# Kernel optimization log

Hardware: AMD Instinct MI355X
Metric: run time of the kernel (lower is better)

The kernel has to match this reference:

```python
import jax, jax.numpy as jnp
import numpy as np

N_NODES = 100000
N_EDGES = 640000
NIN = 128
NOUT = 128


def setup_inputs() -> dict:
    key = jax.random.key(0)
    ks = jax.random.split(key, 10)
    scale = 1.0 / np.sqrt(NIN)
    x = jax.random.normal(ks[0], (N_NODES, NIN), dtype=jnp.float32)
    edge_index = jax.random.randint(ks[1], (2, N_EDGES), 0, N_NODES, dtype=jnp.int64)
    edge_attr = jnp.zeros((N_EDGES, 1), dtype=jnp.float32)
    Wk = jax.random.uniform(ks[2], (NIN, NOUT), jnp.float32, -scale, scale)
    bk = jax.random.uniform(ks[3], (NOUT,), jnp.float32, -scale, scale)
    Wq = jax.random.uniform(ks[4], (NIN, NOUT), jnp.float32, -scale, scale)
    bq = jax.random.uniform(ks[5], (NOUT,), jnp.float32, -scale, scale)
    Wv = jax.random.uniform(ks[6], (NIN, NOUT), jnp.float32, -scale, scale)
    bv = jax.random.uniform(ks[7], (NOUT,), jnp.float32, -scale, scale)
    Wskip = jax.random.uniform(ks[8], (NIN, NOUT), jnp.float32, -scale, scale)
    bias = jax.random.uniform(ks[9], (NOUT,), jnp.float32, -scale, scale)
    return {
        "x": x, "edge_index": edge_index, "edge_attr": edge_attr,
        "Wk": Wk, "bk": bk, "Wq": Wq, "bq": bq,
        "Wv": Wv, "bv": bv, "Wskip": Wskip, "bias": bias,
    }


def reference(x, edge_index, edge_attr, Wk, bk, Wq, bq, Wv, bv, Wskip, bias):
    # PyG ResGatedGraphConv: out_i = W_skip x_i + b + sum_{j->i} sigmoid(k_i + q_j) * v_j
    # k = lin_key(x) (applied to dst), q = lin_query(x) (src), v = lin_value(x) (src)
    src, dst = edge_index[0], edge_index[1]
    k = x @ Wk + bk            # [N, NOUT]
    q = x @ Wq + bq            # [N, NOUT]
    v = x @ Wv + bv            # [N, NOUT]
    eta = jax.nn.sigmoid(k[dst] + q[src])   # [E, NOUT] per-edge gate
    msg = eta * v[src]                       # [E, NOUT]
    agg = jax.ops.segment_sum(msg, dst, num_segments=x.shape[0])  # [N, NOUT]
    return agg + x @ Wskip + bias
```

## Files before the change

### kernel.cpp

```cpp
#include <hip/hip_runtime.h>
#include <hip/hip_bf16.h>

typedef __bf16 v4bf __attribute__((ext_vector_type(4)));
typedef __bf16 v8bf __attribute__((ext_vector_type(8)));
typedef float  v16f __attribute__((ext_vector_type(16)));

__device__ __forceinline__ unsigned short f2bf(float f) {
    union { float f; unsigned int u; } a; a.f = f;
    unsigned int r = a.u + 0x7FFFu + ((a.u >> 16) & 1u);
    return (unsigned short)(r >> 16);
}

__device__ __forceinline__ void unpack8(uint4 rawv, float* f) {
    unsigned int w[4] = { rawv.x, rawv.y, rawv.z, rawv.w };
    #pragma unroll
    for (int i = 0; i < 4; ++i) {
        f[2 * i]     = __uint_as_float(w[i] << 16);
        f[2 * i + 1] = __uint_as_float(w[i] & 0xFFFF0000u);
    }
}

__global__ __launch_bounds__(256) void prep_w(
    const float* __restrict__ Wk, const float* __restrict__ Wq,
    const float* __restrict__ Wv, const float* __restrict__ Ws,
    unsigned short* __restrict__ Wt)
{
    int i = blockIdx.x * 256 + threadIdx.x;
    int m = i >> 14;
    int r = i & 16383;
    int n = r >> 7, k = r & 127;
    const float* W = (m == 0) ? Wk : (m == 1) ? Wq : (m == 2) ? Wv : Ws;
    Wt[i] = f2bf(W[k * 128 + n]);
}

__global__ __launch_bounds__(256) void gemm_one(
    const float* __restrict__ x, int N,
    const unsigned short* __restrict__ Wt,
    const float* __restrict__ bk, const float* __restrict__ bq,
    const float* __restrict__ bv, const float* __restrict__ bs,
    unsigned short* __restrict__ kws, unsigned short* __restrict__ qws,
    unsigned short* __restrict__ vws, float* __restrict__ out)
{
    __shared__ unsigned short wlds[128 * 132];
    const int m = blockIdx.y;
    const unsigned short* wsrc = Wt + m * 16384;
    const int t = threadIdx.x;

    #pragma unroll
    for (int i = 0; i < 8; ++i) {
        int g = t + i * 256;
        int col = g >> 4, ch = g & 15;
        uint4 val = ((const uint4*)wsrc)[g];
        unsigned short* d = wlds + col * 132 + ch * 8;
        *(uint2*)d       = make_uint2(val.x, val.y);
        *(uint2*)(d + 4) = make_uint2(val.z, val.w);
    }

    const int l = t & 63;
    const int w = t >> 6;
    const int r0w = blockIdx.x * 128 + w * 32;
    const int arow = r0w + (l & 31);
    const int kb = (l >> 5) * 8;

    v8bf a[8];
    #pragma unroll
    for (int c = 0; c < 8; ++c) {
        if (arow < N) {
            const float* xp = x + (size_t)arow * 128 + c * 16 + kb;
            float4 u0 = *(const float4*)(xp);
            float4 u1 = *(const float4*)(xp + 4);
            a[c][0] = (__bf16)u0.x; a[c][1] = (__bf16)u0.y;
            a[c][2] = (__bf16)u0.z; a[c][3] = (__bf16)u0.w;
            a[c][4] = (__bf16)u1.x; a[c][5] = (__bf16)u1.y;
            a[c][6] = (__bf16)u1.z; a[c][7] = (__bf16)u1.w;
        } else {
            #pragma unroll
            for (int j = 0; j < 8; ++j) a[c][j] = (__bf16)0.f;
        }
    }

    __syncthreads();

    const float* bvec = (m == 0) ? bk : (m == 1) ? bq : (m == 2) ? bv : bs;
    const int colin = l & 31;
    const int rowb  = 4 * (l >> 5);

    #pragma unroll
    for (int ct = 0; ct < 4; ++ct) {
        const int col = ct * 32 + colin;
        const float bcol = bvec[col];
        const unsigned short* wp = wlds + col * 132 + kb;
        v16f acc = {};
        #pragma unroll
        for (int c = 0; c < 8; ++c) {
            v4bf b0 = *(const v4bf*)(wp + c * 16);
            v4bf b1 = *(const v4bf*)(wp + c * 16 + 4);
            v8bf b = __builtin_shufflevector(b0, b1, 0, 1, 2, 3, 4, 5, 6, 7);
            acc = __builtin_amdgcn_mfma_f32_32x32x16_bf16(a[c], b, acc, 0, 0, 0);
        }
        if (m == 3) {
            #pragma unroll
            for (int reg = 0; reg < 16; ++reg) {
                int row = r0w + rowb + (reg & 3) + 8 * (reg >> 2);
                if (row < N) out[(size_t)row * 128 + col] = acc[reg] + bcol;
            }
        } else {
            unsigned short* dst = (m == 0) ? kws : (m == 1) ? qws : vws;
            #pragma unroll
            for (int reg = 0; reg < 16; ++reg) {
                int row = r0w + rowb + (reg & 3) + 8 * (reg >> 2);
                if (row < N) dst[(size_t)row * 128 + col] = f2bf(acc[reg] + bcol);
            }
        }
    }
}


__global__ __launch_bounds__(256) void zero_ints(int* __restrict__ p, int n) {
    int i = blockIdx.x * 256 + threadIdx.x;
    if (i < n) p[i] = 0;
}

__global__ __launch_bounds__(256) void count_deg(
    const int* __restrict__ ei, int E, int* __restrict__ deg)
{
    int e = blockIdx.x * 256 + threadIdx.x;
    if (e >= E) return;
    atomicAdd(&deg[ei[E + e]], 1);
}

__global__ __launch_bounds__(256) void scan_chunks(
    const int* __restrict__ deg, int N, int* __restrict__ rowStart,
    int* __restrict__ chunkTot)
{
    __shared__ int sums[256];
    const int t = threadIdx.x;
    const int base = blockIdx.x * 1024 + t * 4;
    int d0 = 0, d1 = 0, d2 = 0, d3 = 0;
    if (base + 3 < N) {
        int4 dd = *(const int4*)(deg + base);
        d0 = dd.x; d1 = dd.y; d2 = dd.z; d3 = dd.w;
    } else {
        if (base + 0 < N) d0 = deg[base + 0];
        if (base + 1 < N) d1 = deg[base + 1];
        if (base + 2 < N) d2 = deg[base + 2];
        if (base + 3 < N) d3 = deg[base + 3];
    }
    int tot = d0 + d1 + d2 + d3;
    sums[t] = tot;
    __syncthreads();
    #pragma unroll
    for (int off = 1; off < 256; off <<= 1) {
        int v = (t >= off) ? sums[t - off] : 0;
        __syncthreads();
        sums[t] += v;
        __syncthreads();
    }
    int excl = sums[t] - tot;
    if (base + 0 < N) rowStart[base + 0] = excl;
    if (base + 1 < N) rowStart[base + 1] = excl + d0;
    if (base + 2 < N) rowStart[base + 2] = excl + d0 + d1;
    if (base + 3 < N) rowStart[base + 3] = excl + d0 + d1 + d2;
    if (t == 255) chunkTot[blockIdx.x] = sums[255];
}

__global__ __launch_bounds__(128) void scan_tops(
    const int* __restrict__ chunkTot, int* __restrict__ chunkOff, int nChunks)
{
    __shared__ int s[128];
    int t = threadIdx.x;
    int v = (t < nChunks) ? chunkTot[t] : 0;
    s[t] = v;
    __syncthreads();
    #pragma unroll
    for (int off = 1; off < 128; off <<= 1) {
        int u = (t >= off) ? s[t - off] : 0;
        __syncthreads();
        s[t] += u;
        __syncthreads();
    }
    if (t < nChunks) chunkOff[t] = s[t] - v;
}

__global__ __launch_bounds__(256) void add_offsets(
    int* __restrict__ rowStart, int* __restrict__ rowEnd,
    const int* __restrict__ chunkOff, int N)
{
    int i = blockIdx.x * 256 + threadIdx.x;
    if (i >= N) return;
    int v = rowStart[i] + chunkOff[i >> 10];
    rowStart[i] = v;
    rowEnd[i] = v;
}

__global__ __launch_bounds__(256) void fill_csr(
    const int* __restrict__ ei, int E,
    int* __restrict__ rowEnd, int* __restrict__ elist)
{
    int e = blockIdx.x * 256 + threadIdx.x;
    if (e >= E) return;
    int s = ei[e];
    int d = ei[E + e];
    int pos = atomicAdd(&rowEnd[d], 1);
    elist[pos] = s;
}

__global__ __launch_bounds__(256) void gather_agg(
    const int* __restrict__ rowStart, const int* __restrict__ rowEnd,
    const int* __restrict__ elist,
    const unsigned short* __restrict__ kws,
    const unsigned short* __restrict__ qws,
    const unsigned short* __restrict__ vws,
    float* __restrict__ out, int N)
{
    int gid = blockIdx.x * 256 + threadIdx.x;
    int node = gid >> 4;
    if (node >= N) return;
    int fo = (gid & 15) << 3;

    float kf[8];
    unpack8(*(const uint4*)(kws + (size_t)node * 128 + fo), kf);
    float acc[8] = {};

    int p = rowStart[node];
    const int e = rowEnd[node];

    for (; p + 2 <= e; p += 2) {
        int s0 = elist[p];
        int s1 = elist[p + 1];
        uint4 q0r = *(const uint4*)(qws + (size_t)s0 * 128 + fo);
        uint4 v0r = *(const uint4*)(vws + (size_t)s0 * 128 + fo);
        uint4 q1r = *(const uint4*)(qws + (size_t)s1 * 128 + fo);
        uint4 v1r = *(const uint4*)(vws + (size_t)s1 * 128 + fo);
        float qf0[8], vf0[8], qf1[8], vf1[8];
        unpack8(q0r, qf0); unpack8(v0r, vf0);
        unpack8(q1r, qf1); unpack8(v1r, vf1);
        #pragma unroll
        for (int j = 0; j < 8; ++j) {
            float e0 = __fdividef(1.f, 1.f + __expf(-(kf[j] + qf0[j])));
            float e1 = __fdividef(1.f, 1.f + __expf(-(kf[j] + qf1[j])));
            acc[j] = fmaf(e0, vf0[j], acc[j]);
            acc[j] = fmaf(e1, vf1[j], acc[j]);
        }
    }
    if (p < e) {
        int s0 = elist[p];
        uint4 q0r = *(const uint4*)(qws + (size_t)s0 * 128 + fo);
        uint4 v0r = *(const uint4*)(vws + (size_t)s0 * 128 + fo);
        float qf0[8], vf0[8];
        unpack8(q0r, qf0); unpack8(v0r, vf0);
        #pragma unroll
        for (int j = 0; j < 8; ++j) {
            float e0 = __fdividef(1.f, 1.f + __expf(-(kf[j] + qf0[j])));
            acc[j] = fmaf(e0, vf0[j], acc[j]);
        }
    }

    float* orow = out + (size_t)node * 128 + fo;
    float4 o0 = *(float4*)(orow);
    float4 o1 = *(float4*)(orow + 4);
    o0.x += acc[0]; o0.y += acc[1]; o0.z += acc[2]; o0.w += acc[3];
    o1.x += acc[4]; o1.y += acc[5]; o1.z += acc[6]; o1.w += acc[7];
    *(float4*)(orow)     = o0;
    *(float4*)(orow + 4) = o1;
}

extern "C" void kernel_launch(void* const* d_in, const int* in_sizes, int n_in,
                              void* d_out, int out_size, void* d_ws, size_t ws_size,
                              hipStream_t stream) {
    const float* x    = (const float*)d_in[0];
    const int*   ei   = (const int*)d_in[1];
    const float* Wk   = (const float*)d_in[3];
    const float* bk   = (const float*)d_in[4];
    const float* Wq   = (const float*)d_in[5];
    const float* bq   = (const float*)d_in[6];
    const float* Wv   = (const float*)d_in[7];
    const float* bv   = (const float*)d_in[8];
    const float* Ws   = (const float*)d_in[9];
    const float* bias = (const float*)d_in[10];

    const int N = in_sizes[0] / 128;
    const int E = in_sizes[1] / 2;
    float* out = (float*)d_out;

    unsigned short* kws = (unsigned short*)d_ws;
    unsigned short* qws = kws + (size_t)N * 128;
    unsigned short* vws = qws + (size_t)N * 128;
    int* deg      = (int*)(vws + (size_t)N * 128);
    int* rowStart = deg + N;
    int* rowEnd   = rowStart + N;
    int* chunkTot = rowEnd + N;
    int* chunkOff = chunkTot + 128;
    int* elist    = chunkOff + 128;
    unsigned short* Wt = (unsigned short*)(elist + E);

    const int nChunks = (N + 1023) / 1024;

    prep_w<<<256, 256, 0, stream>>>(Wk, Wq, Wv, Ws, Wt);
    dim3 g1((N + 127) / 128, 4);
    gemm_one<<<g1, 256, 0, stream>>>(
        x, N, Wt, bk, bq, bv, bias, kws, qws, vws, out);

    zero_ints<<<(N + 255) / 256, 256, 0, stream>>>(deg, N);
    count_deg<<<(E + 255) / 256, 256, 0, stream>>>(ei, E, deg);
    scan_chunks<<<nChunks, 256, 0, stream>>>(deg, N, rowStart, chunkTot);
    scan_tops<<<1, 128, 0, stream>>>(chunkTot, chunkOff, nChunks);
    add_offsets<<<(N + 255) / 256, 256, 0, stream>>>(rowStart, rowEnd, chunkOff, N);
    fill_csr<<<(E + 255) / 256, 256, 0, stream>>>(ei, E, rowEnd, elist);

    gather_agg<<<((size_t)N * 16 + 255) / 256, 256, 0, stream>>>(
        rowStart, rowEnd, elist, kws, qws, vws, out, N);
}
```

Baseline: 317.4 us.

## Fuse projection GEMMs into persistent kernel, merge small CSR kernels, unroll gather by four

The GEMM becomes a persistent 1024-thread kernel where each of 16 waves holds one weight/column tile in registers. x is read once per 32-row tile, staged as bf16 in shared memory and prefetched for the next tile, instead of being read four times (once per projection). The deg zeroing is folded into the weight-prep kernel, and the top-level scan is folded into add_offsets, removing two launches. The gather loop is unrolled to four edges to keep more loads in flight, at the cost of extra registers.

```diff
diff --git a/kernel.cpp b/kernel.cpp
--- a/kernel.cpp
+++ b/kernel.cpp
@@ -20,20 +20,23 @@
     }
 }
 
-__global__ __launch_bounds__(256) void prep_w(
+__global__ __launch_bounds__(256) void prep_w_zero(
     const float* __restrict__ Wk, const float* __restrict__ Wq,
     const float* __restrict__ Wv, const float* __restrict__ Ws,
-    unsigned short* __restrict__ Wt)
+    unsigned short* __restrict__ Wt, int* __restrict__ deg, int N)
 {
     int i = blockIdx.x * 256 + threadIdx.x;
-    int m = i >> 14;
-    int r = i & 16383;
-    int n = r >> 7, k = r & 127;
-    const float* W = (m == 0) ? Wk : (m == 1) ? Wq : (m == 2) ? Wv : Ws;
-    Wt[i] = f2bf(W[k * 128 + n]);
-}
-
-__global__ __launch_bounds__(256) void gemm_one(
+    if (i < 65536) {
+        int m = i >> 14;
+        int r = i & 16383;
+        int n = r >> 7, k = r & 127;
+        const float* W = (m == 0) ? Wk : (m == 1) ? Wq : (m == 2) ? Wv : Ws;
+        Wt[i] = f2bf(W[k * 128 + n]);
+    }
+    if (i < N) deg[i] = 0;
+}
+
+__global__ __launch_bounds__(1024, 4) void gemm_fused(
     const float* __restrict__ x, int N,
     const unsigned short* __restrict__ Wt,
     const float* __restrict__ bk, const float* __restrict__ bq,
@@ -41,85 +44,90 @@
     unsigned short* __restrict__ kws, unsigned short* __restrict__ qws,
     unsigned short* __restrict__ vws, float* __restrict__ out)
 {
-    __shared__ unsigned short wlds[128 * 132];
-    const int m = blockIdx.y;
-    const unsigned short* wsrc = Wt + m * 16384;
-    const int t = threadIdx.x;
-
-    #pragma unroll
-    for (int i = 0; i < 8; ++i) {
-        int g = t + i * 256;
-        int col = g >> 4, ch = g & 15;
-        uint4 val = ((const uint4*)wsrc)[g];
-        unsigned short* d = wlds + col * 132 + ch * 8;
-        *(uint2*)d       = make_uint2(val.x, val.y);
-        *(uint2*)(d + 4) = make_uint2(val.z, val.w);
-    }
-
-    const int l = t & 63;
-    const int w = t >> 6;
-    const int r0w = blockIdx.x * 128 + w * 32;
-    const int arow = r0w + (l & 31);
-    const int kb = (l >> 5) * 8;
-
-    v8bf a[8];
-    #pragma unroll
-    for (int c = 0; c < 8; ++c) {
-        if (arow < N) {
-            const float* xp = x + (size_t)arow * 128 + c * 16 + kb;
-            float4 u0 = *(const float4*)(xp);
-            float4 u1 = *(const float4*)(xp + 4);
-            a[c][0] = (__bf16)u0.x; a[c][1] = (__bf16)u0.y;
-            a[c][2] = (__bf16)u0.z; a[c][3] = (__bf16)u0.w;
-            a[c][4] = (__bf16)u1.x; a[c][5] = (__bf16)u1.y;
-            a[c][6] = (__bf16)u1.z; a[c][7] = (__bf16)u1.w;
-        } else {
+    __shared__ __align__(16) unsigned short xs[32 * 132];
+    const int t   = threadIdx.x;
+    const int wid = t >> 6;
+    const int m   = wid >> 2;
+    const int ct  = wid & 3;
+    const int l   = t & 63;
+    const int col = ct * 32 + (l & 31);
+    const int kb  = (l >> 5) * 8;
+
+    v8bf b[8];
+    {
+        const unsigned short* wp = Wt + m * 16384 + col * 128 + kb;
+        #pragma unroll
+        for (int c = 0; c < 8; ++c) b[c] = *(const v8bf*)(wp + c * 16);
+    }
+    const float* bvec = (m == 0) ? bk : (m == 1) ? bq : (m == 2) ? bv : bs;
+    const float bcol = bvec[col];
+    unsigned short* dst = (m == 0) ? kws : (m == 1) ? qws : vws;
+
+    const int srow = t >> 5;
+    const int sk4  = (t & 31) << 2;
+    const int rowb = 4 * (l >> 5);
+
+    const int ntiles = (N + 31) >> 5;
+    int tile = blockIdx.x;
+    if (tile >= ntiles) return;
+
+    float4 stg = make_float4(0.f, 0.f, 0.f, 0.f);
+    {
+        int gr = tile * 32 + srow;
+        if (gr < N) stg = *(const float4*)(x + (size_t)gr * 128 + sk4);
+    }
+
+    while (true) {
+        ushort4 pk;
+        pk.x = f2bf(stg.x); pk.y = f2bf(stg.y);
+        pk.z = f2bf(stg.z); pk.w = f2bf(stg.w);
+        *(ushort4*)(xs + srow * 132 + sk4) = pk;
+        __syncthreads();
+
+        v8bf a[8];
+        {
+            const unsigned short* ap = xs + (l & 31) * 132 + kb;
             #pragma unroll
-            for (int j = 0; j < 8; ++j) a[c][j] = (__bf16)0.f;
+            for (int c = 0; c < 8; ++c) {
+                v4bf a0 = *(const v4bf*)(ap + c * 16);
+                v4bf a1 = *(const v4bf*)(ap + c * 16 + 4);
+                a[c] = __builtin_shufflevector(a0, a1, 0, 1, 2, 3, 4, 5, 6, 7);
+            }
         }
-    }
-
-    __syncthreads();
-
-    const float* bvec = (m == 0) ? bk : (m == 1) ? bq : (m == 2) ? bv : bs;
-    const int colin = l & 31;
-    const int rowb  = 4 * (l >> 5);
-
-    #pragma unroll
-    for (int ct = 0; ct < 4; ++ct) {
-        const int col = ct * 32 + colin;
-        const float bcol = bvec[col];
-        const unsigned short* wp = wlds + col * 132 + kb;
+
+        int next = tile + gridDim.x;
+        if (next < ntiles) {
+            int gr = next * 32 + srow;
+            stg = (gr < N) ? *(const float4*)(x + (size_t)gr * 128 + sk4)
+                           : make_float4(0.f, 0.f, 0.f, 0.f);
+        }
+
         v16f acc = {};
         #pragma unroll
-        for (int c = 0; c < 8; ++c) {
-            v4bf b0 = *(const v4bf*)(wp + c * 16);
-            v4bf b1 = *(const v4bf*)(wp + c * 16 + 4);
-            v8bf b = __builtin_shufflevector(b0, b1, 0, 1, 2, 3, 4, 5, 6, 7);
-            acc = __builtin_amdgcn_mfma_f32_32x32x16_bf16(a[c], b, acc, 0, 0, 0);
-        }
+        for (int c = 0; c < 8; ++c)
+            acc = __builtin_amdgcn_mfma_f32_32x32x16_bf16(a[c], b[c], acc, 0, 0, 0);
+
+        const int r0 = tile * 32 + rowb;
         if (m == 3) {
             #pragma unroll
             for (int reg = 0; reg < 16; ++reg) {
-                int row = r0w + rowb + (reg & 3) + 8 * (reg >> 2);
+                int row = r0 + (reg & 3) + 8 * (reg >> 2);
                 if (row < N) out[(size_t)row * 128 + col] = acc[reg] + bcol;
             }
         } else {
-            unsigned short* dst = (m == 0) ? kws : (m == 1) ? qws : vws;
             #pragma unroll
             for (int reg = 0; reg < 16; ++reg) {
-                int row = r0w + rowb + (reg & 3) + 8 * (reg >> 2);
+                int row = r0 + (reg & 3) + 8 * (reg >> 2);
                 if (row < N) dst[(size_t)row * 128 + col] = f2bf(acc[reg] + bcol);
             }
         }
-    }
-}
-
-
-__global__ __launch_bounds__(256) void zero_ints(int* __restrict__ p, int n) {
-    int i = blockIdx.x * 256 + threadIdx.x;
-    if (i < n) p[i] = 0;
-}
+
+        tile = next;
+        if (tile >= ntiles) break;
+        __syncthreads();
+    }
+}
+
 
 __global__ __launch_bounds__(256) void count_deg(
     const int* __restrict__ ei, int E, int* __restrict__ deg)
@@ -164,33 +172,39 @@
     if (t == 255) chunkTot[blockIdx.x] = sums[255];
 }
 
-__global__ __launch_bounds__(128) void scan_tops(
-    const int* __restrict__ chunkTot, int* __restrict__ chunkOff, int nChunks)
+__global__ __launch_bounds__(256) void add_offsets(
+    int* __restrict__ rowStart, int* __restrict__ rowEnd,
+    const int* __restrict__ chunkTot, int N, int nChunks)
 {
     __shared__ int s[128];
-    int t = threadIdx.x;
-    int v = (t < nChunks) ? chunkTot[t] : 0;
-    s[t] = v;
+    const int t = threadIdx.x;
+    if (t < 128) s[t] = (t < nChunks) ? chunkTot[t] : 0;
     __syncthreads();
     #pragma unroll
     for (int off = 1; off < 128; off <<= 1) {
-        int u = (t >= off) ? s[t - off] : 0;
-        __syncthreads();
-        s[t] += u;
-        __syncthreads();
-    }
-    if (t < nChunks) chunkOff[t] = s[t] - v;
-}
-
-__global__ __launch_bounds__(256) void add_offsets(
-    int* __restrict__ rowStart, int* __restrict__ rowEnd,
-    const int* __restrict__ chunkOff, int N)
-{
-    int i = blockIdx.x * 256 + threadIdx.x;
-    if (i >= N) return;
-    int v = rowStart[i] + chunkOff[i >> 10];
-    rowStart[i] = v;
-    rowEnd[i] = v;
+        int u = 0;
+        if (t < 128 && t >= off) u = s[t - off];
+        __syncthreads();
+        if (t < 128) s[t] += u;
+        __syncthreads();
+    }
+    const int coff = (blockIdx.x == 0) ? 0 : s[blockIdx.x - 1];
+    const int base = blockIdx.x * 1024 + t * 4;
+    if (base + 3 < N) {
+        int4 r = *(const int4*)(rowStart + base);
+        r.x += coff; r.y += coff; r.z += coff; r.w += coff;
+        *(int4*)(rowStart + base) = r;
+        *(int4*)(rowEnd + base) = r;
+    } else {
+        #pragma unroll
+        for (int j = 0; j < 4; ++j) {
+            if (base + j < N) {
+                int v = rowStart[base + j] + coff;
+                rowStart[base + j] = v;
+                rowEnd[base + j] = v;
+            }
+        }
+    }
 }
 
 __global__ __launch_bounds__(256) void fill_csr(
@@ -225,35 +239,43 @@
     int p = rowStart[node];
     const int e = rowEnd[node];
 
-    for (; p + 2 <= e; p += 2) {
-        int s0 = elist[p];
-        int s1 = elist[p + 1];
+    for (; p + 4 <= e; p += 4) {
+        int s0 = elist[p], s1 = elist[p + 1], s2 = elist[p + 2], s3 = elist[p + 3];
         uint4 q0r = *(const uint4*)(qws + (size_t)s0 * 128 + fo);
         uint4 v0r = *(const uint4*)(vws + (size_t)s0 * 128 + fo);
         uint4 q1r = *(const uint4*)(qws + (size_t)s1 * 128 + fo);
         uint4 v1r = *(const uint4*)(vws + (size_t)s1 * 128 + fo);
-        float qf0[8], vf0[8], qf1[8], vf1[8];
-        unpack8(q0r, qf0); unpack8(v0r, vf0);
-        unpack8(q1r, qf1); unpack8(v1r, vf1);
-        #pragma unroll
-        for (int j = 0; j < 8; ++j) {
-            float e0 = __fdividef(1.f, 1.f + __expf(-(kf[j] + qf0[j])));
-            float e1 = __fdividef(1.f, 1.f + __expf(-(kf[j] + qf1[j])));
-            acc[j] = fmaf(e0, vf0[j], acc[j]);
-            acc[j] = fmaf(e1, vf1[j], acc[j]);
-        }
-    }
-    if (p < e) {
+        uint4 q2r = *(const uint4*)(qws + (size_t)s2 * 128 + fo);
+        uint4 v2r = *(const uint4*)(vws + (size_t)s2 * 128 + fo);
+        uint4 q3r = *(const uint4*)(qws + (size_t)s3 * 128 + fo);
+        uint4 v3r = *(const uint4*)(vws + (size_t)s3 * 128 + fo);
+        float qf[8], vf[8];
+        unpack8(q0r, qf); unpack8(v0r, vf);
+        #pragma unroll
+        for (int j = 0; j < 8; ++j)
+            acc[j] = fmaf(__fdividef(1.f, 1.f + __expf(-(kf[j] + qf[j]))), vf[j], acc[j]);
+        unpack8(q1r, qf); unpack8(v1r, vf);
+        #pragma unroll
+        for (int j = 0; j < 8; ++j)
+            acc[j] = fmaf(__fdividef(1.f, 1.f + __expf(-(kf[j] + qf[j]))), vf[j], acc[j]);
+        unpack8(q2r, qf); unpack8(v2r, vf);
+        #pragma unroll
+        for (int j = 0; j < 8; ++j)
+            acc[j] = fmaf(__fdividef(1.f, 1.f + __expf(-(kf[j] + qf[j]))), vf[j], acc[j]);
+        unpack8(q3r, qf); unpack8(v3r, vf);
+        #pragma unroll
+        for (int j = 0; j < 8; ++j)
+            acc[j] = fmaf(__fdividef(1.f, 1.f + __expf(-(kf[j] + qf[j]))), vf[j], acc[j]);
+    }
+    for (; p < e; ++p) {
         int s0 = elist[p];
         uint4 q0r = *(const uint4*)(qws + (size_t)s0 * 128 + fo);
         uint4 v0r = *(const uint4*)(vws + (size_t)s0 * 128 + fo);
-        float qf0[8], vf0[8];
-        unpack8(q0r, qf0); unpack8(v0r, vf0);
-        #pragma unroll
-        for (int j = 0; j < 8; ++j) {
-            float e0 = __fdividef(1.f, 1.f + __expf(-(kf[j] + qf0[j])));
-            acc[j] = fmaf(e0, vf0[j], acc[j]);
-        }
+        float qf[8], vf[8];
+        unpack8(q0r, qf); unpack8(v0r, vf);
+        #pragma unroll
+        for (int j = 0; j < 8; ++j)
+            acc[j] = fmaf(__fdividef(1.f, 1.f + __expf(-(kf[j] + qf[j]))), vf[j], acc[j]);
     }
 
     float* orow = out + (size_t)node * 128 + fo;
@@ -290,22 +312,18 @@
     int* rowStart = deg + N;
     int* rowEnd   = rowStart + N;
     int* chunkTot = rowEnd + N;
-    int* chunkOff = chunkTot + 128;
-    int* elist    = chunkOff + 128;
+    int* elist    = chunkTot + 128;
     unsigned short* Wt = (unsigned short*)(elist + E);
 
     const int nChunks = (N + 1023) / 1024;
 
-    prep_w<<<256, 256, 0, stream>>>(Wk, Wq, Wv, Ws, Wt);
-    dim3 g1((N + 127) / 128, 4);
-    gemm_one<<<g1, 256, 0, stream>>>(
+    prep_w_zero<<<512, 256, 0, stream>>>(Wk, Wq, Wv, Ws, Wt, deg, N);
+    gemm_fused<<<512, 1024, 0, stream>>>(
         x, N, Wt, bk, bq, bv, bias, kws, qws, vws, out);
 
-    zero_ints<<<(N + 255) / 256, 256, 0, stream>>>(deg, N);
     count_deg<<<(E + 255) / 256, 256, 0, stream>>>(ei, E, deg);
     scan_chunks<<<nChunks, 256, 0, stream>>>(deg, N, rowStart, chunkTot);
-    scan_tops<<<1, 128, 0, stream>>>(chunkTot, chunkOff, nChunks);
-    add_offsets<<<(N + 255) / 256, 256, 0, stream>>>(rowStart, rowEnd, chunkOff, N);
+    add_offsets<<<nChunks, 256, 0, stream>>>(rowStart, rowEnd, chunkTot, N, nChunks);
     fill_csr<<<(E + 255) / 256, 256, 0, stream>>>(ei, E, rowEnd, elist);
 
     gather_agg<<<((size_t)N * 16 + 255) / 256, 256, 0, stream>>>(
```

Result: faster. 308.7 us (-2.7%).
